# Performance work log

Hardware: AMD Instinct MI355X
Metric: run time of the kernel (lower is better)

The kernel has to match this reference:

```python
import jax, jax.numpy as jnp
import numpy as np

YOLO_INPUT_SIZE = 416.0
SCORE_THRESHOLD = 0.5
IOU_THRESHOLD = 0.45
AREA_THRESHOLD = 0.0005
MAX_OUTPUT_BOXES = 10
NEG = -1e9


def setup_inputs() -> dict:
    key = jax.random.key(0)
    y = jax.random.uniform(key, (64, 10647, 85), dtype=jnp.float32)
    # first 4 channels are xywh in input-pixel units (YOLO decode divides by 416)
    y = y.at[..., 0:2].multiply(YOLO_INPUT_SIZE)          # centers in [0, 416)
    y = y.at[..., 2:4].multiply(YOLO_INPUT_SIZE * 0.3)    # w,h up to ~125 px
    return {"y_pred": y}


def _decode(y_pred):
    flat = y_pred.reshape(-1, y_pred.shape[-1])           # [N, 85]
    box, conf, probs = flat[:, :4], flat[:, 4], flat[:, 5:]
    scores = conf * jnp.max(probs, axis=-1)               # [N]
    classes = jnp.argmax(probs, axis=-1).astype(jnp.int32)
    b = jnp.clip(box / YOLO_INPUT_SIZE, 0.0, 1.0)
    x, y, w, h = b[:, 0], b[:, 1], b[:, 2], b[:, 3]
    x1 = jnp.clip(x - w * 0.5, 0.0, 1.0)
    y1 = jnp.clip(y - h * 0.5, 0.0, 1.0)
    x2 = jnp.clip(x + w * 0.5, 0.0, 1.0)
    y2 = jnp.clip(y + h * 0.5, 0.0, 1.0)
    big_enough = (x2 - x1) * (y2 - y1) > AREA_THRESHOLD
    keep = big_enough & (scores > SCORE_THRESHOLD)
    boxes = jnp.stack([x1, y1, x2, y2], axis=-1)          # [N, 4]
    work = jnp.where(keep, scores, NEG)                   # masked working scores
    return boxes, scores, classes, work


def _iou_one_vs_all(ref, boxes):
    ix1 = jnp.maximum(ref[0], boxes[:, 0])
    iy1 = jnp.maximum(ref[1], boxes[:, 1])
    ix2 = jnp.minimum(ref[2], boxes[:, 2])
    iy2 = jnp.minimum(ref[3], boxes[:, 3])
    inter = jnp.maximum(ix2 - ix1, 0.0) * jnp.maximum(iy2 - iy1, 0.0)
    a_ref = (ref[2] - ref[0]) * (ref[3] - ref[1])
    a_all = (boxes[:, 2] - boxes[:, 0]) * (boxes[:, 3] - boxes[:, 1])
    return inter / (a_ref + a_all - inter + 1e-10)


def _greedy_nms(boxes, work):
    def step(w, _):
        j = jnp.argmax(w)
        v = w[j] > SCORE_THRESHOLD
        iou = _iou_one_vs_all(boxes[j], boxes)
        w = jnp.where(v & (iou > IOU_THRESHOLD), NEG, w)
        w = w.at[j].set(NEG)
        return w, (j.astype(jnp.int32), v)
    _, (idxs, valid) = jax.lax.scan(step, work, None, length=MAX_OUTPUT_BOXES)
    return idxs, valid


def reference(y_pred):
    boxes, scores, classes, work = _decode(y_pred)
    idxs, valid = _greedy_nms(boxes, work)
    # fixed-size (padded) outputs instead of dynamic boolean gather; `valid`
    # marks real detections (original returns only the valid rows)
    sel_boxes = boxes[idxs]                # [10, 4]
    sel_scores = scores[idxs][:, None]     # [10, 1]
    sel_classes = classes[idxs][:, None]   # [10, 1]
    return sel_boxes, sel_scores, sel_classes, valid
```

## Files before the change

kernel.cpp:

```cpp
#include <hip/hip_runtime.h>

#define ROWS   681408
#define NBINS  8192
#define CAP    64
#define TOPK   192
#define SELCAP 256

#define WS_ROW0     4
#define WS_CNT      16
#define WS_BUCKET   8448

__device__ __forceinline__ float clip01(float v) {
    return fminf(fmaxf(v, 0.0f), 1.0f);
}

__global__ void init_kernel(unsigned int* __restrict__ ws) {
    int i = blockIdx.x * 256 + threadIdx.x;
    if (i < NBINS) ws[WS_CNT + i] = 0u;
}

__global__ __launch_bounds__(256) void decode_kernel(
    const float* __restrict__ y, unsigned int* __restrict__ ws)
{
    const int t    = threadIdx.x;
    const int lane = t & 63;
    const int wave = t >> 6;
    const int g    = lane >> 4;
    const int s    = lane & 15;
    const int row  = blockIdx.x * 16 + wave * 4 + g;

    const float*  p  = y + (size_t)row * 85;
    const float2* p2 = (const float2*)p;

    float2 A = p2[s];
    float2 B = p2[s + 16];
    float c0 = -1.0f, c1 = -1.0f;
    if (s < 10) { float2 C = p2[s + 32]; c0 = C.x; c1 = C.y; }
    else if (s == 10) { c0 = p[84]; }

    float bv = -1.0f; int bc = 1 << 20;
    {
        int e = 2 * s;
        if (e >= 5 && A.x > bv) { bv = A.x; bc = e - 5; }
        if (e + 1 >= 5 && A.y > bv) { bv = A.y; bc = e - 4; }
        if (B.x > bv) { bv = B.x; bc = e + 27; }
        if (B.y > bv) { bv = B.y; bc = e + 28; }
        if (e + 64 <= 84 && c0 > bv) { bv = c0; bc = e + 59; }
        if (e + 65 <= 84 && c1 > bv) { bv = c1; bc = e + 60; }
    }

    #pragma unroll
    for (int m = 8; m >= 1; m >>= 1) {
        float ov = __shfl_xor(bv, m, 64);
        int   oc = __shfl_xor(bc, m, 64);
        if (ov > bv || (ov == bv && oc < bc)) { bv = ov; bc = oc; }
    }

    const int gb = lane & 48;
    float bx = __shfl(A.x, gb + 0, 64);
    float by = __shfl(A.y, gb + 0, 64);
    float bw = __shfl(A.x, gb + 1, 64);
    float bh = __shfl(A.y, gb + 1, 64);
    float cf = __shfl(A.x, gb + 2, 64);

    if (s == 0) {
        float score = cf * bv;
        float x  = clip01(bx / 416.0f);
        float yy = clip01(by / 416.0f);
        float w  = clip01(bw / 416.0f);
        float h  = clip01(bh / 416.0f);
        float x1 = clip01(x  - w * 0.5f);
        float y1 = clip01(yy - h * 0.5f);
        float x2 = clip01(x  + w * 0.5f);
        float y2 = clip01(yy + h * 0.5f);
        bool keep = (((x2 - x1) * (y2 - y1)) > 0.0005f) && (score > 0.5f);
        if (keep) {
            int bin = (int)((score - 0.5f) * (2.0f * (float)NBINS));
            bin = min(max(bin, 0), NBINS - 1);
            unsigned int pos = atomicAdd(&ws[WS_CNT + bin], 1u);
            if (pos < (unsigned int)CAP) {
                uint2* bucket = (uint2*)&ws[WS_BUCKET];
                bucket[bin * CAP + pos] =
                    make_uint2(__float_as_uint(score), (unsigned int)row);
            }
        }
        if (row == 0) {
            float* r0 = (float*)&ws[WS_ROW0];
            r0[0] = score; r0[1] = (float)bc;
            r0[2] = x1; r0[3] = y1; r0[4] = x2; r0[5] = y2;
        }
    }
}

__global__ __launch_bounds__(256) void nms_kernel(
    const float* __restrict__ y, unsigned int* __restrict__ ws,
    float* __restrict__ out)
{
    __shared__ unsigned int chunk[256];
    __shared__ unsigned int fine[32];
    __shared__ unsigned long long keys[SELCAP];
    __shared__ float4 sboxes[SELCAP];
    __shared__ int s_coarse;
    __shared__ int s_bstar;
    __shared__ unsigned int s_m;
    __shared__ int s_picks;
    __shared__ unsigned int s_idx[10];
    __shared__ float s_score[10];
    __shared__ float4 s_box[10];
    __shared__ int s_cls[10];

    const int t = threadIdx.x;
    const uint2* bucket = (const uint2*)&ws[WS_BUCKET];

    unsigned int ssum = 0;
    {
        const uint4* cnt4 = (const uint4*)&ws[WS_CNT];
        #pragma unroll
        for (int i = 0; i < 8; i++) {
            uint4 v = cnt4[t * 8 + i];
            ssum += min(v.x, (unsigned int)CAP) + min(v.y, (unsigned int)CAP)
                  + min(v.z, (unsigned int)CAP) + min(v.w, (unsigned int)CAP);
        }
    }
    chunk[t] = ssum;
    for (int i = t; i < SELCAP; i += 256) keys[i] = 0ull;
    if (t == 0) s_m = 0u;
    __syncthreads();

    for (int off = 1; off < 256; off <<= 1) {
        unsigned int v = chunk[t];
        unsigned int a = (t + off < 256) ? chunk[t + off] : 0u;
        __syncthreads();
        chunk[t] = v + a;
        __syncthreads();
    }
    const unsigned int total  = chunk[0];
    const unsigned int target = (total < (unsigned int)TOPK) ? total
                                                             : (unsigned int)TOPK;

    if (target > 0) {
        if (chunk[t] >= target && (t == 255 || chunk[t + 1] < target))
            s_coarse = t;
        __syncthreads();

        const int cb = s_coarse * 32;
        if (t < 32) fine[t] = min(ws[WS_CNT + cb + t], (unsigned int)CAP);
        __syncthreads();
        for (int off = 1; off < 32; off <<= 1) {
            unsigned int v = 0, a = 0;
            if (t < 32) { v = fine[t]; a = (t + off < 32) ? fine[t + off] : 0u; }
            __syncthreads();
            if (t < 32) fine[t] = v + a;
            __syncthreads();
        }
        const unsigned int base = (s_coarse < 255) ? chunk[s_coarse + 1] : 0u;
        if (t < 32) {
            unsigned int sfx = base + fine[t];
            unsigned int nxt = (t == 31) ? base : base + fine[t + 1];
            if (sfx >= target && nxt < target) s_bstar = cb + t;
        }
    } else {
        if (t == 0) s_bstar = NBINS;
    }
    __syncthreads();

    for (int bin = s_bstar + t; bin < NBINS; bin += 256) {
        unsigned int c = ws[WS_CNT + bin];
        if (c > (unsigned int)CAP) c = CAP;
        for (unsigned int j = 0; j < c; j++) {
            uint2 cv = bucket[bin * CAP + j];
            unsigned int pos = atomicAdd(&s_m, 1u);
            if (pos < (unsigned int)SELCAP)
                keys[pos] = ((unsigned long long)cv.x << 32) |
                            (unsigned long long)(0xFFFFFFFFu - cv.y);
        }
    }
    __syncthreads();
    unsigned int M = s_m;
    if (M > (unsigned int)SELCAP) M = SELCAP;

    for (int k = 2; k <= SELCAP; k <<= 1) {
        for (int j = k >> 1; j > 0; j >>= 1) {
            for (int i = t; i < SELCAP; i += 256) {
                int ixj = i ^ j;
                if (ixj > i) {
                    unsigned long long a = keys[i], b = keys[ixj];
                    bool descSeg = ((i & k) == 0);
                    if (descSeg ? (a < b) : (a > b)) { keys[i] = b; keys[ixj] = a; }
                }
            }
            __syncthreads();
        }
    }

    for (int i = t; i < (int)M; i += 256) {
        unsigned int idx = 0xFFFFFFFFu - (unsigned int)(keys[i] & 0xFFFFFFFFull);
        const float* p = y + (size_t)idx * 85;
        float x  = clip01(p[0] / 416.0f);
        float yy = clip01(p[1] / 416.0f);
        float w  = clip01(p[2] / 416.0f);
        float h  = clip01(p[3] / 416.0f);
        sboxes[i] = make_float4(clip01(x - w * 0.5f), clip01(yy - h * 0.5f),
                                clip01(x + w * 0.5f), clip01(yy + h * 0.5f));
    }
    __syncthreads();

    if (t == 0) {
        int np = 0;
        for (int i = 0; i < (int)M && np < 10; i++) {
            float4 b = sboxes[i];
            bool ok = true;
            for (int kk = 0; kk < np; kk++) {
                float4 r = s_box[kk];
                float ix1 = fmaxf(r.x, b.x);
                float iy1 = fmaxf(r.y, b.y);
                float ix2 = fminf(r.z, b.z);
                float iy2 = fminf(r.w, b.w);
                float inter = fmaxf(ix2 - ix1, 0.0f) * fmaxf(iy2 - iy1, 0.0f);
                float aref = (r.z - r.x) * (r.w - r.y);
                float aall = (b.z - b.x) * (b.w - b.y);
                float iou = inter / (aref + aall - inter + 1e-10f);
                if (iou > 0.45f) { ok = false; break; }
            }
            if (ok) {
                s_box[np] = b;
                s_idx[np] = 0xFFFFFFFFu - (unsigned int)(keys[i] & 0xFFFFFFFFull);
                s_score[np] = __uint_as_float((unsigned int)(keys[i] >> 32));
                np++;
            }
        }
        s_picks = np;
    }
    __syncthreads();

    {
        int p = t >> 4, s = t & 15;
        float bv = -1.0f; int bc = 1 << 20;
        if (p < s_picks) {
            const float* pr = y + (size_t)s_idx[p] * 85 + 5;
            #pragma unroll
            for (int kk = 0; kk < 5; kk++) {
                float v = pr[s + 16 * kk];
                int c = s + 16 * kk;
                if (v > bv) { bv = v; bc = c; }
            }
        }
        #pragma unroll
        for (int m = 8; m >= 1; m >>= 1) {
            float ov = __shfl_xor(bv, m, 64);
            int   oc = __shfl_xor(bc, m, 64);
            if (ov > bv || (ov == bv && oc < bc)) { bv = ov; bc = oc; }
        }
        if (p < s_picks && s == 0) s_cls[p] = bc;
    }
    __syncthreads();

    if (t == 0) {
        const float* r0 = (const float*)&ws[WS_ROW0];
        float score0 = r0[0], class0 = r0[1];
        float4 box0 = make_float4(r0[2], r0[3], r0[4], r0[5]);
        for (int kk = 0; kk < 10; kk++) {
            bool v = kk < s_picks;
            float4 b = v ? s_box[kk] : box0;
            out[4 * kk + 0] = b.x;
            out[4 * kk + 1] = b.y;
            out[4 * kk + 2] = b.z;
            out[4 * kk + 3] = b.w;
            out[40 + kk] = v ? s_score[kk] : score0;
            out[50 + kk] = v ? (float)s_cls[kk] : class0;
            out[60 + kk] = v ? 1.0f : 0.0f;
        }
    }
}

extern "C" void kernel_launch(void* const* d_in, const int* in_sizes, int n_in,
                              void* d_out, int out_size, void* d_ws, size_t ws_size,
                              hipStream_t stream)
{
    const float* y = (const float*)d_in[0];
    unsigned int* ws = (unsigned int*)d_ws;

    init_kernel<<<dim3(NBINS / 256), dim3(256), 0, stream>>>(ws);
    decode_kernel<<<dim3(ROWS / 16), dim3(256), 0, stream>>>(y, ws);
    nms_kernel<<<dim3(1), dim3(256), 0, stream>>>(y, ws, (float*)d_out);
}
```

Before: 78.09 us.

## Decode one row per thread with float4 loads instead of 16-lane groups

The decode kernel now gives each thread a whole 85-float row. It reads the row with 21 float4 loads plus one scalar load and runs the class argmax serially in registers. This drops the cross-lane shuffle reduction and the idle lanes that only loaded data, and it shrinks the grid by 16x. In exchange, adjacent threads read addresses 340 bytes apart, so each wave load touches many cache lines. The float4 loads are also only 4-byte aligned because the row stride is not a multiple of 16 bytes.

Measured after the change: 85.07 us. 8.9% more time.

```diff
diff --git a/kernel.cpp b/kernel.cpp
--- a/kernel.cpp
+++ b/kernel.cpp
@@ -22,73 +22,57 @@
 __global__ __launch_bounds__(256) void decode_kernel(
     const float* __restrict__ y, unsigned int* __restrict__ ws)
 {
-    const int t    = threadIdx.x;
-    const int lane = t & 63;
-    const int wave = t >> 6;
-    const int g    = lane >> 4;
-    const int s    = lane & 15;
-    const int row  = blockIdx.x * 16 + wave * 4 + g;
+    const int row = blockIdx.x * 256 + threadIdx.x;
+    if (row >= ROWS) return;
 
     const float*  p  = y + (size_t)row * 85;
-    const float2* p2 = (const float2*)p;
-
-    float2 A = p2[s];
-    float2 B = p2[s + 16];
-    float c0 = -1.0f, c1 = -1.0f;
-    if (s < 10) { float2 C = p2[s + 32]; c0 = C.x; c1 = C.y; }
-    else if (s == 10) { c0 = p[84]; }
-
-    float bv = -1.0f; int bc = 1 << 20;
+    const float4* p4 = (const float4*)p;
+
+    float4 f0 = p4[0];
+    float4 f1 = p4[1];
+    const float cf = f1.x;
+
+    float bv = f1.y; int bc = 0;
+    if (f1.z > bv) { bv = f1.z; bc = 1; }
+    if (f1.w > bv) { bv = f1.w; bc = 2; }
+    #pragma unroll
+    for (int j = 2; j <= 20; j++) {
+        float4 f = p4[j];
+        const int b0 = 4 * j - 5;
+        if (f.x > bv) { bv = f.x; bc = b0; }
+        if (f.y > bv) { bv = f.y; bc = b0 + 1; }
+        if (f.z > bv) { bv = f.z; bc = b0 + 2; }
+        if (f.w > bv) { bv = f.w; bc = b0 + 3; }
+    }
     {
-        int e = 2 * s;
-        if (e >= 5 && A.x > bv) { bv = A.x; bc = e - 5; }
-        if (e + 1 >= 5 && A.y > bv) { bv = A.y; bc = e - 4; }
-        if (B.x > bv) { bv = B.x; bc = e + 27; }
-        if (B.y > bv) { bv = B.y; bc = e + 28; }
-        if (e + 64 <= 84 && c0 > bv) { bv = c0; bc = e + 59; }
-        if (e + 65 <= 84 && c1 > bv) { bv = c1; bc = e + 60; }
-    }
-
-    #pragma unroll
-    for (int m = 8; m >= 1; m >>= 1) {
-        float ov = __shfl_xor(bv, m, 64);
-        int   oc = __shfl_xor(bc, m, 64);
-        if (ov > bv || (ov == bv && oc < bc)) { bv = ov; bc = oc; }
-    }
-
-    const int gb = lane & 48;
-    float bx = __shfl(A.x, gb + 0, 64);
-    float by = __shfl(A.y, gb + 0, 64);
-    float bw = __shfl(A.x, gb + 1, 64);
-    float bh = __shfl(A.y, gb + 1, 64);
-    float cf = __shfl(A.x, gb + 2, 64);
-
-    if (s == 0) {
-        float score = cf * bv;
-        float x  = clip01(bx / 416.0f);
-        float yy = clip01(by / 416.0f);
-        float w  = clip01(bw / 416.0f);
-        float h  = clip01(bh / 416.0f);
-        float x1 = clip01(x  - w * 0.5f);
-        float y1 = clip01(yy - h * 0.5f);
-        float x2 = clip01(x  + w * 0.5f);
-        float y2 = clip01(yy + h * 0.5f);
-        bool keep = (((x2 - x1) * (y2 - y1)) > 0.0005f) && (score > 0.5f);
-        if (keep) {
-            int bin = (int)((score - 0.5f) * (2.0f * (float)NBINS));
-            bin = min(max(bin, 0), NBINS - 1);
-            unsigned int pos = atomicAdd(&ws[WS_CNT + bin], 1u);
-            if (pos < (unsigned int)CAP) {
-                uint2* bucket = (uint2*)&ws[WS_BUCKET];
-                bucket[bin * CAP + pos] =
-                    make_uint2(__float_as_uint(score), (unsigned int)row);
-            }
-        }
-        if (row == 0) {
-            float* r0 = (float*)&ws[WS_ROW0];
-            r0[0] = score; r0[1] = (float)bc;
-            r0[2] = x1; r0[3] = y1; r0[4] = x2; r0[5] = y2;
-        }
+        float e84 = p[84];
+        if (e84 > bv) { bv = e84; bc = 79; }
+    }
+
+    const float score = cf * bv;
+    float x  = clip01(f0.x / 416.0f);
+    float yy = clip01(f0.y / 416.0f);
+    float w  = clip01(f0.z / 416.0f);
+    float h  = clip01(f0.w / 416.0f);
+    float x1 = clip01(x  - w * 0.5f);
+    float y1 = clip01(yy - h * 0.5f);
+    float x2 = clip01(x  + w * 0.5f);
+    float y2 = clip01(yy + h * 0.5f);
+    bool keep = (((x2 - x1) * (y2 - y1)) > 0.0005f) && (score > 0.5f);
+    if (keep) {
+        int bin = (int)((score - 0.5f) * (2.0f * (float)NBINS));
+        bin = min(max(bin, 0), NBINS - 1);
+        unsigned int pos = atomicAdd(&ws[WS_CNT + bin], 1u);
+        if (pos < (unsigned int)CAP) {
+            uint2* bucket = (uint2*)&ws[WS_BUCKET];
+            bucket[bin * CAP + pos] =
+                make_uint2(__float_as_uint(score), (unsigned int)row);
+        }
+    }
+    if (row == 0) {
+        float* r0 = (float*)&ws[WS_ROW0];
+        r0[0] = score; r0[1] = (float)bc;
+        r0[2] = x1; r0[3] = y1; r0[4] = x2; r0[5] = y2;
     }
 }
 
@@ -281,6 +265,6 @@
     unsigned int* ws = (unsigned int*)d_ws;
 
     init_kernel<<<dim3(NBINS / 256), dim3(256), 0, stream>>>(ws);
-    decode_kernel<<<dim3(ROWS / 16), dim3(256), 0, stream>>>(y, ws);
+    decode_kernel<<<dim3((ROWS + 255) / 256), dim3(256), 0, stream>>>(y, ws);
     nms_kernel<<<dim3(1), dim3(256), 0, stream>>>(y, ws, (float*)d_out);
 }
```
